# Performance work log

Hardware: AMD Instinct MI355X
Metric: run time of the kernel (lower is better)

Reference implementation:

```python
import jax, jax.numpy as jnp
import numpy as np

E = 2048   # embedding_size
H = 2048   # hidden_size
B = 512    # batch
OUT = 2    # output_size (coords)


def setup_inputs() -> dict:
    key = jax.random.key(0)
    ks = jax.random.split(key, 11)
    s = 0.02
    return {
        "embedding": jax.random.normal(ks[0], (B, E), dtype=jnp.float32),
        "max_seq_length": 256,
        "W_embed": jax.random.normal(ks[1], (H, E), dtype=jnp.float32) * s,
        "b_embed": jnp.zeros((H,), dtype=jnp.float32),
        "W_ih": jax.random.normal(ks[2], (4 * H, OUT), dtype=jnp.float32) * s,
        "b_ih": jnp.zeros((4 * H,), dtype=jnp.float32),
        "W_hh": jax.random.normal(ks[3], (4 * H, H), dtype=jnp.float32) * s,
        "b_hh": jnp.zeros((4 * H,), dtype=jnp.float32),
        "W_out": jax.random.normal(ks[4], (OUT, H), dtype=jnp.float32) * s,
        "b_out": jnp.zeros((OUT,), dtype=jnp.float32),
        "W_stop": jax.random.normal(ks[5], (1, H), dtype=jnp.float32) * s,
        "b_stop": jnp.zeros((1,), dtype=jnp.float32),
    }


def reference(embedding, max_seq_length, W_embed, b_embed, W_ih, b_ih,
              W_hh, b_hh, W_out, b_out, W_stop, b_stop):
    # h_0 from embedding head (num_layers == 1)
    h0 = embedding @ W_embed.T + b_embed          # (B, H)
    c0 = jnp.zeros_like(h0)
    x0 = jnp.zeros((embedding.shape[0], OUT), dtype=embedding.dtype)

    def step(carry, _):
        h, c, x = carry
        gates = x @ W_ih.T + b_ih + h @ W_hh.T + b_hh    # (B, 4H)
        i, f, g, o = jnp.split(gates, 4, axis=-1)         # torch gate order i,f,g,o
        c = jax.nn.sigmoid(f) * c + jax.nn.sigmoid(i) * jnp.tanh(g)
        h = jax.nn.sigmoid(o) * jnp.tanh(c)
        coord = h @ W_out.T + b_out                        # (B, 2)
        stop = jax.nn.sigmoid(h @ W_stop.T + b_stop)       # (B, 1)
        return (h, c, coord), (coord, stop)

    _, (coords, stops) = jax.lax.scan(step, (h0, c0, x0), xs=None,
                                      length=max_seq_length)
    outputs = jnp.transpose(coords, (1, 0, 2))     # (B, T, 2)
    stop_probs = jnp.transpose(stops, (1, 0, 2))   # (B, T, 1)
    return outputs, stop_probs
```

## Files before the change

kernel.cpp:

```cpp
#include <hip/hip_runtime.h>
#include <stdint.h>

#define E_DIM 2048
#define H_DIM 2048
#define B_DIM 512
#define T_DIM 256
#define G4H   8192

typedef unsigned short u16;
typedef __attribute__((ext_vector_type(8))) short bf16x8;
typedef __attribute__((ext_vector_type(4))) float f32x4;

__device__ inline u16 f2b(float f) {
  union { float f; uint32_t i; } v; v.f = f;
  uint32_t u = v.i;
  return (u16)((u + 0x7FFFu + ((u >> 16) & 1u)) >> 16);
}
__device__ inline float b2f(u16 u) {
  union { uint32_t i; float f; } v; v.i = ((uint32_t)u) << 16; return v.f;
}

__device__ __forceinline__ void stage16(const void* g, void* l) {
  __builtin_amdgcn_global_load_lds(
      (const __attribute__((address_space(1))) uint32_t*)g,
      (__attribute__((address_space(3))) uint32_t*)l, 16, 0, 0);
}

__global__ __launch_bounds__(256) void convert_bf16(const float* __restrict__ s,
                                                    u16* __restrict__ d, int n4) {
  int i = blockIdx.x * 256 + threadIdx.x;
  if (i < n4) {
    float4 f = ((const float4*)s)[i];
    ushort4 o;
    o.x = f2b(f.x); o.y = f2b(f.y); o.z = f2b(f.z); o.w = f2b(f.w);
    ((ushort4*)d)[i] = o;
  }
}

__global__ __launch_bounds__(256) void build_weff(const float* __restrict__ W,
                                                  const float* __restrict__ W_ih,
                                                  const float* __restrict__ W_out,
                                                  u16* __restrict__ Wz) {
  int id = blockIdx.x * 256 + threadIdx.x;
  int lane = id & 63;
  int k32  = (id >> 6) & 63;
  int n16  = id >> 12;
  int np = n16 * 16 + (lane & 15);
  int k  = k32 * 32 + (lane >> 4) * 8;
  int g = np & 3, jrow = np >> 2;
  int src = g * H_DIM + jrow;
  float wi0 = W_ih[src * 2 + 0], wi1 = W_ih[src * 2 + 1];
  const float* sw = W + (size_t)src * H_DIM + k;
  u16 out[8];
  for (int j = 0; j < 8; ++j) {
    float v = sw[j] + wi0 * W_out[k + j] + wi1 * W_out[H_DIM + k + j];
    out[j] = f2b(v);
  }
  u16* dst = Wz + (size_t)id * 8;
  *(ushort4*)(dst) = *(ushort4*)&out[0];
  *(ushort4*)(dst + 4) = *(ushort4*)&out[4];
}

__global__ __launch_bounds__(256) void build_epi(const float* __restrict__ b_ih,
                                                 const float* __restrict__ b_hh,
                                                 const float* __restrict__ W_ih,
                                                 const float* __restrict__ b_out,
                                                 float* __restrict__ epi) {
  int np = blockIdx.x * 256 + threadIdx.x;
  int src = (np & 3) * H_DIM + (np >> 2);
  float wi0 = W_ih[src * 2 + 0], wi1 = W_ih[src * 2 + 1];
  float4 e;
  e.x = b_ih[src] + b_hh[src] + b_out[0] * wi0 + b_out[1] * wi1;
  e.y = wi0;
  e.z = wi1;
  e.w = 0.f;
  ((float4*)epi)[np] = e;
}

#define BM 64
#define BN 128
#define BK 32
__global__ __launch_bounds__(256) void gemm_bt(const u16* __restrict__ A,
                                               const u16* __restrict__ Bm,
                                               float* __restrict__ C,
                                               int M, int N, int K) {
  __shared__ u16 sA[BM * BK];
  __shared__ u16 sB[BN * BK];
  const int t = threadIdx.x;
  const int bm0 = blockIdx.y * BM, bn0 = blockIdx.x * BN;
  const int wave = t >> 6, lane = t & 63;
  const int wm = (wave >> 1) * 32, wn = (wave & 1) * 64;
  const int r16 = lane & 15, quad = lane >> 4;

  f32x4 acc[2][4];
  const f32x4 z = {0.f, 0.f, 0.f, 0.f};
  for (int i = 0; i < 2; ++i)
    for (int j = 0; j < 4; ++j) acc[i][j] = z;

  const int arow = t >> 2, acg = t & 3;

  for (int k0 = 0; k0 < K; k0 += BK) {
    __syncthreads();
    *(uint4*)&sA[arow * BK + acg * 8] =
        *(const uint4*)&A[(size_t)(bm0 + arow) * K + k0 + acg * 8];
    for (int i = 0; i < 2; ++i) {
      int c = t + 256 * i;
      int row = c >> 2, cg = c & 3;
      *(uint4*)&sB[row * BK + cg * 8] =
          *(const uint4*)&Bm[(size_t)(bn0 + row) * K + k0 + cg * 8];
    }
    __syncthreads();
    bf16x8 af[2], bfr[4];
    for (int mt = 0; mt < 2; ++mt)
      af[mt] = *(const bf16x8*)&sA[(wm + mt * 16 + r16) * BK + quad * 8];
    for (int nt = 0; nt < 4; ++nt)
      bfr[nt] = *(const bf16x8*)&sB[(wn + nt * 16 + r16) * BK + quad * 8];
    for (int mt = 0; mt < 2; ++mt)
      for (int nt = 0; nt < 4; ++nt)
        acc[mt][nt] = __builtin_amdgcn_mfma_f32_16x16x32_bf16(af[mt], bfr[nt],
                                                              acc[mt][nt], 0, 0, 0);
  }
  for (int mt = 0; mt < 2; ++mt)
    for (int nt = 0; nt < 4; ++nt) {
      int row = bm0 + wm + mt * 16 + quad * 4;
      int col = bn0 + wn + nt * 16 + r16;
      for (int r = 0; r < 4; ++r)
        C[(size_t)(row + r) * N + col] = acc[mt][nt][r];
    }
}

__global__ __launch_bounds__(256) void init_state(const float* __restrict__ h0pre,
                                                  const float* __restrict__ b_embed,
                                                  u16* __restrict__ h,
                                                  float* __restrict__ c,
                                                  float* __restrict__ xzero) {
  int idx = blockIdx.x * 256 + threadIdx.x;
  int bg = idx >> 11, k = idx & (H_DIM - 1);
  float v = h0pre[idx] + b_embed[k];
  size_t chunk = (((size_t)(bg >> 4)) * 64 + (k >> 5)) * 64 + ((k >> 3) & 3) * 16 + (bg & 15);
  size_t pos = chunk * 8 + (k & 7);
  h[pos] = f2b(v);
  c[pos] = 0.f;
  if (idx < B_DIM * 2) xzero[idx] = 0.f;
}

__global__ __launch_bounds__(64) void calc_xcorr(const float* __restrict__ h0pre,
                                                 const float* __restrict__ b_embed,
                                                 const float* __restrict__ W_out,
                                                 const float* __restrict__ b_out,
                                                 float* __restrict__ xc) {
  int m = blockIdx.x, ln = threadIdx.x;
  float s0 = 0.f, s1 = 0.f;
  for (int k = ln; k < H_DIM; k += 64) {
    float hv = h0pre[(size_t)m * H_DIM + k] + b_embed[k];
    s0 += hv * W_out[k];
    s1 += hv * W_out[H_DIM + k];
  }
  for (int off = 32; off > 0; off >>= 1) {
    s0 += __shfl_down(s0, off);
    s1 += __shfl_down(s1, off);
  }
  if (ln == 0) {
    xc[m * 2 + 0] = -(s0 + b_out[0]);
    xc[m * 2 + 1] = -(s1 + b_out[1]);
  }
}

__global__ __launch_bounds__(256) void init_out(const float* __restrict__ b_out,
                                                const float* __restrict__ b_stop,
                                                float* __restrict__ coords,
                                                float* __restrict__ stops) {
  int i = blockIdx.x * 256 + threadIdx.x;
  coords[i * 2 + 0] = b_out[0];
  coords[i * 2 + 1] = b_out[1];
  stops[i] = b_stop[0];
}

__global__ __launch_bounds__(256) void finalize_stops(float* __restrict__ stops) {
  int i = blockIdx.x * 256 + threadIdx.x;
  stops[i] = 1.f / (1.f + __expf(-stops[i]));
}

__global__ __launch_bounds__(512, 2) void gemm_lstm(const u16* __restrict__ hA,
                                                 const u16* __restrict__ Wz,
                                                 const float* __restrict__ epi,
                                                 const float* __restrict__ x,
                                                 float* __restrict__ c,
                                                 u16* __restrict__ h_out,
                                                 const float* __restrict__ W_out,
                                                 const float* __restrict__ W_stop,
                                                 float* __restrict__ coords,
                                                 float* __restrict__ stops,
                                                 int trow) {
  __shared__ __align__(16) char smem[131072];

  const int bid = blockIdx.x;
  const int nt = (bid & 7) * 8 + ((bid >> 3) & 7);
  const int mt = bid >> 6;

  const int t = threadIdx.x, wv = t >> 6, ln = t & 63;
  const int kq = wv >> 1, wn = wv & 1;
  const int r16 = ln & 15, quad = ln >> 4;

  const u16* Bb[4];
#pragma unroll
  for (int ni = 0; ni < 4; ++ni)
    Bb[ni] = Wz + ((size_t)(nt * 8 + wn * 4 + ni) * 64) * 512 + ln * 8;
  const int kbase = kq * 16;

  const u16* Ag[8];
  uint32_t Aoff[8];
#pragma unroll
  for (int s = 0; s < 8; ++s) {
    int ti = wv * 8 + s;
    int kq_s = ti >> 4, kloc_s = (ti >> 3) & 1, m16i = ti & 7;
    Ag[s] = hA + ((size_t)(mt * 8 + m16i) * 64 + kq_s * 16 + kloc_s) * 512 + ln * 8;
    Aoff[s] = (uint32_t)(kq_s * 16384 + kloc_s * 8192 + m16i * 1024);
  }

  f32x4 acc[8][4];
  const f32x4 z = {0.f, 0.f, 0.f, 0.f};
#pragma unroll
  for (int i = 0; i < 8; ++i)
#pragma unroll
    for (int j = 0; j < 4; ++j) acc[i][j] = z;

#pragma unroll
  for (int s = 0; s < 8; ++s) stage16(Ag[s], smem + Aoff[s]);
  __builtin_amdgcn_sched_barrier(0);
  bf16x8 bfr[2][4];
#pragma unroll
  for (int d = 0; d < 2; ++d)
#pragma unroll
    for (int ni = 0; ni < 4; ++ni)
      bfr[d][ni] = *(const bf16x8*)(Bb[ni] + (size_t)(kbase + d) * 512);

  const uint32_t ln16 = (uint32_t)(ln * 16);
  const uint32_t rdk = (uint32_t)(kq * 16384);

  for (int it = 0; it < 8; ++it) {
    asm volatile("s_waitcnt vmcnt(8)" ::: "memory");
    __builtin_amdgcn_s_barrier();
    const uint32_t bb = (uint32_t)((it & 1) * 65536);
    if (it < 7) {
#pragma unroll
      for (int s = 0; s < 8; ++s)
        stage16(Ag[s] + (size_t)(it + 1) * 1024, smem + ((bb ^ 65536) + Aoff[s]));
      __builtin_amdgcn_sched_barrier(0);
    }
#pragma unroll
    for (int kloc = 0; kloc < 2; ++kloc) {
      const char* rb = smem + bb + rdk + (uint32_t)(kloc * 8192);
      bf16x8 af[8];
#pragma unroll
      for (int mi = 0; mi < 8; ++mi)
        af[mi] = *(const bf16x8*)(rb + mi * 1024 + ln16);
      __builtin_amdgcn_s_setprio(1);
#pragma unroll
      for (int mi = 0; mi < 8; ++mi)
#pragma unroll
        for (int ni = 0; ni < 4; ++ni)
          acc[mi][ni] = __builtin_amdgcn_mfma_f32_16x16x32_bf16(
              af[mi], bfr[kloc][ni], acc[mi][ni], 0, 0, 0);
      __builtin_amdgcn_s_setprio(0);
      const int knext = it * 2 + kloc + 2;
      if (knext < 16) {
#pragma unroll
        for (int ni = 0; ni < 4; ++ni)
          bfr[kloc][ni] = *(const bf16x8*)(Bb[ni] + (size_t)(kbase + knext) * 512);
      }
    }
  }
  __syncthreads();

  float* cb = (float*)smem;
  if (kq >= 2) {
    float* dst = cb + ((kq - 2) * 2 + wn) * 8192;
#pragma unroll
    for (int mi = 0; mi < 8; ++mi)
#pragma unroll
      for (int ni = 0; ni < 4; ++ni)
        *(f32x4*)&dst[((mi * 4 + ni) * 64 + ln) * 4] = acc[mi][ni];
  }
  __syncthreads();
  if (kq < 2) {
    const float* src = cb + (kq * 2 + wn) * 8192;
#pragma unroll
    for (int mi = 0; mi < 8; ++mi)
#pragma unroll
      for (int ni = 0; ni < 4; ++ni)
        acc[mi][ni] += *(const f32x4*)&src[((mi * 4 + ni) * 64 + ln) * 4];
  }
  __syncthreads();
  if (kq == 1) {
    float* dst = cb + wn * 8192;
#pragma unroll
    for (int mi = 0; mi < 8; ++mi)
#pragma unroll
      for (int ni = 0; ni < 4; ++ni)
        *(f32x4*)&dst[((mi * 4 + ni) * 64 + ln) * 4] = acc[mi][ni];
  }
  __syncthreads();
  if (kq == 0) {
    const float* src = cb + wn * 8192;
#pragma unroll
    for (int mi = 0; mi < 8; ++mi)
#pragma unroll
      for (int ni = 0; ni < 4; ++ni)
        acc[mi][ni] += *(const f32x4*)&src[((mi * 4 + ni) * 64 + ln) * 4];
  }
  __syncthreads();

  float* gt = (float*)smem;
  if (kq == 0) {
#pragma unroll
    for (int mi = 0; mi < 8; ++mi)
#pragma unroll
      for (int ni = 0; ni < 4; ++ni) {
        int row = mi * 16 + quad * 4;
        int col = wn * 64 + ni * 16 + r16;
        f32x4 v = acc[mi][ni];
#pragma unroll
        for (int r = 0; r < 4; ++r)
          gt[(row + r) * 132 + col] = v[r];
      }
  }
  __syncthreads();

  {
    const int lrow = wv * 16 + r16;
    const int bg = mt * 128 + lrow;
    const float x0 = x[bg * 2 + 0], x1 = x[bg * 2 + 1];
    const size_t chunk = (((size_t)(bg >> 4)) * 64 + nt) * 64 + ln;
    const int hc0 = nt * 32 + quad * 8;
    float cv[8]; u16 hv[8];
    float s0 = 0.f, s1 = 0.f, s2 = 0.f;
    const float4* epi4 = (const float4*)epi;
    f32x4 cold0 = *(const f32x4*)&c[chunk * 8 + 0];
    f32x4 cold1 = *(const f32x4*)&c[chunk * 8 + 4];
#pragma unroll
    for (int j = 0; j < 8; ++j) {
      int col = quad * 32 + j * 4;
      float4 g4 = *(const float4*)&gt[lrow * 132 + col];
      float4 e0 = epi4[nt * 128 + col + 0];
      float4 e1 = epi4[nt * 128 + col + 1];
      float4 e2 = epi4[nt * 128 + col + 2];
      float4 e3 = epi4[nt * 128 + col + 3];
      float gi = g4.x + e0.x + x0 * e0.y + x1 * e0.z;
      float gf = g4.y + e1.x + x0 * e1.y + x1 * e1.z;
      float gg = g4.z + e2.x + x0 * e2.y + x1 * e2.z;
      float go = g4.w + e3.x + x0 * e3.y + x1 * e3.z;
      float si = 1.f / (1.f + __expf(-gi));
      float sf = 1.f / (1.f + __expf(-gf));
      float so = 1.f / (1.f + __expf(-go));
      float cold = (j < 4) ? cold0[j & 3] : cold1[j & 3];
      float cn = sf * cold + si * tanhf(gg);
      cv[j] = cn;
      float hf = so * tanhf(cn);
      hv[j] = f2b(hf);
      s0 += hf * W_out[hc0 + j];
      s1 += hf * W_out[H_DIM + hc0 + j];
      s2 += hf * W_stop[hc0 + j];
    }
    *(float4*)&c[chunk * 8 + 0] = *(float4*)&cv[0];
    *(float4*)&c[chunk * 8 + 4] = *(float4*)&cv[4];
    *(ushort4*)&h_out[chunk * 8 + 0] = *(ushort4*)&hv[0];
    *(ushort4*)&h_out[chunk * 8 + 4] = *(ushort4*)&hv[4];
    s0 += __shfl_xor(s0, 16); s1 += __shfl_xor(s1, 16); s2 += __shfl_xor(s2, 16);
    s0 += __shfl_xor(s0, 32); s1 += __shfl_xor(s1, 32); s2 += __shfl_xor(s2, 32);
    if (quad == 0) {
      atomicAdd(&coords[((size_t)bg * T_DIM + trow) * 2 + 0], s0);
      atomicAdd(&coords[((size_t)bg * T_DIM + trow) * 2 + 1], s1);
      atomicAdd(&stops[(size_t)bg * T_DIM + trow], s2);
    }
  }
}

extern "C" void kernel_launch(void* const* d_in, const int* in_sizes, int n_in,
                              void* d_out, int out_size, void* d_ws, size_t ws_size,
                              hipStream_t stream) {
  const float* embedding = (const float*)d_in[0];
  const float* W_embed   = (const float*)d_in[2];
  const float* b_embed   = (const float*)d_in[3];
  const float* W_ih      = (const float*)d_in[4];
  const float* b_ih      = (const float*)d_in[5];
  const float* W_hh      = (const float*)d_in[6];
  const float* b_hh      = (const float*)d_in[7];
  const float* W_out     = (const float*)d_in[8];
  const float* b_out     = (const float*)d_in[9];
  const float* W_stop    = (const float*)d_in[10];
  const float* b_stop    = (const float*)d_in[11];

  float* coords = (float*)d_out;
  float* stops  = (float*)d_out + (size_t)B_DIM * T_DIM * 2;

  char* ws = (char*)d_ws;
  u16* W_z     = (u16*)ws;   ws += (size_t)G4H * H_DIM * 2;
  u16* W_emb_b = (u16*)ws;   ws += (size_t)H_DIM * E_DIM * 2;
  u16* emb_b   = (u16*)ws;   ws += (size_t)B_DIM * E_DIM * 2;
  float* h0pre = (float*)ws; ws += (size_t)B_DIM * H_DIM * 4;
  float* epi   = (float*)ws; ws += (size_t)G4H * 4 * 4;
  float* cbuf  = (float*)ws; ws += (size_t)B_DIM * H_DIM * 4;
  u16* hbuf0   = (u16*)ws;   ws += (size_t)B_DIM * H_DIM * 2;
  u16* hbuf1   = (u16*)ws;   ws += (size_t)B_DIM * H_DIM * 2;
  float* xcorr = (float*)ws; ws += (size_t)B_DIM * 2 * 4;
  float* xzero = (float*)ws; ws += (size_t)B_DIM * 2 * 4;

  convert_bf16<<<(B_DIM * E_DIM / 4 + 255) / 256, 256, 0, stream>>>(embedding, emb_b, B_DIM * E_DIM / 4);
  convert_bf16<<<(H_DIM * E_DIM / 4 + 255) / 256, 256, 0, stream>>>(W_embed, W_emb_b, H_DIM * E_DIM / 4);
  build_weff<<<(G4H * H_DIM / 8) / 256, 256, 0, stream>>>(W_hh, W_ih, W_out, W_z);
  build_epi<<<G4H / 256, 256, 0, stream>>>(b_ih, b_hh, W_ih, b_out, epi);
  init_out<<<(B_DIM * T_DIM) / 256, 256, 0, stream>>>(b_out, b_stop, coords, stops);

  gemm_bt<<<dim3(H_DIM / BN, B_DIM / BM), 256, 0, stream>>>(emb_b, W_emb_b, h0pre,
                                                            B_DIM, H_DIM, E_DIM);
  init_state<<<(B_DIM * H_DIM) / 256, 256, 0, stream>>>(h0pre, b_embed, hbuf0, cbuf, xzero);
  calc_xcorr<<<B_DIM, 64, 0, stream>>>(h0pre, b_embed, W_out, b_out, xcorr);

  for (int t = 0; t < T_DIM; ++t) {
    u16* h_in  = (t & 1) ? hbuf1 : hbuf0;
    u16* h_out = (t & 1) ? hbuf0 : hbuf1;
    const float* xv = (t == 0) ? xcorr : xzero;
    gemm_lstm<<<256, 512, 0, stream>>>(h_in, W_z, epi, xv, cbuf, h_out,
                                       W_out, W_stop, coords, stops, t);
  }
  finalize_stops<<<(B_DIM * T_DIM) / 256, 256, 0, stream>>>(stops);
}
```

Before: 7.600 ms.

## Fuse all LSTM timesteps into one persistent cooperative kernel with grid barrier

Replaces the 256 per-timestep gemm_lstm launches with a single cooperative persistent kernel that loops over time and synchronises all 256 blocks through an atomic-counter grid barrier. The cell state now stays in registers instead of being reloaded from and stored to global memory each step, and the zero-x buffer is dropped. This removes per-launch overhead and the c-state traffic. In exchange it adds a spin barrier per step and requires all 256 blocks to be co-resident.

```diff
diff --git a/kernel.cpp b/kernel.cpp
--- a/kernel.cpp
+++ b/kernel.cpp
@@ -131,17 +131,13 @@
 
 __global__ __launch_bounds__(256) void init_state(const float* __restrict__ h0pre,
                                                   const float* __restrict__ b_embed,
-                                                  u16* __restrict__ h,
-                                                  float* __restrict__ c,
-                                                  float* __restrict__ xzero) {
+                                                  u16* __restrict__ h) {
   int idx = blockIdx.x * 256 + threadIdx.x;
   int bg = idx >> 11, k = idx & (H_DIM - 1);
   float v = h0pre[idx] + b_embed[k];
   size_t chunk = (((size_t)(bg >> 4)) * 64 + (k >> 5)) * 64 + ((k >> 3) & 3) * 16 + (bg & 15);
   size_t pos = chunk * 8 + (k & 7);
   h[pos] = f2b(v);
-  c[pos] = 0.f;
-  if (idx < B_DIM * 2) xzero[idx] = 0.f;
 }
 
 __global__ __launch_bounds__(64) void calc_xcorr(const float* __restrict__ h0pre,
@@ -181,24 +177,20 @@
   stops[i] = 1.f / (1.f + __expf(-stops[i]));
 }
 
-__global__ __launch_bounds__(512, 2) void gemm_lstm(const u16* __restrict__ hA,
-                                                 const u16* __restrict__ Wz,
-                                                 const float* __restrict__ epi,
-                                                 const float* __restrict__ x,
-                                                 float* __restrict__ c,
-                                                 u16* __restrict__ h_out,
-                                                 const float* __restrict__ W_out,
-                                                 const float* __restrict__ W_stop,
-                                                 float* __restrict__ coords,
-                                                 float* __restrict__ stops,
-                                                 int trow) {
+__global__ __launch_bounds__(512, 2) void gemm_lstm_all(
+    u16* __restrict__ hb0, u16* __restrict__ hb1,
+    const u16* __restrict__ Wz, const float* __restrict__ epi,
+    const float* __restrict__ xcorr,
+    const float* __restrict__ W_out, const float* __restrict__ W_stop,
+    float* __restrict__ coords, float* __restrict__ stops,
+    unsigned int* __restrict__ bar) {
   __shared__ __align__(16) char smem[131072];
 
   const int bid = blockIdx.x;
   const int nt = (bid & 7) * 8 + ((bid >> 3) & 7);
   const int mt = bid >> 6;
 
-  const int t = threadIdx.x, wv = t >> 6, ln = t & 63;
+  const int tid = threadIdx.x, wv = tid >> 6, ln = tid & 63;
   const int kq = wv >> 1, wn = wv & 1;
   const int r16 = ln & 15, quad = ln >> 4;
 
@@ -208,170 +200,193 @@
     Bb[ni] = Wz + ((size_t)(nt * 8 + wn * 4 + ni) * 64) * 512 + ln * 8;
   const int kbase = kq * 16;
 
-  const u16* Ag[8];
-  uint32_t Aoff[8];
+  uint32_t Aoffe[8], Aoff[8];
 #pragma unroll
   for (int s = 0; s < 8; ++s) {
     int ti = wv * 8 + s;
     int kq_s = ti >> 4, kloc_s = (ti >> 3) & 1, m16i = ti & 7;
-    Ag[s] = hA + ((size_t)(mt * 8 + m16i) * 64 + kq_s * 16 + kloc_s) * 512 + ln * 8;
+    Aoffe[s] = (uint32_t)((((mt * 8 + m16i) * 64 + kq_s * 16 + kloc_s) * 512) + ln * 8);
     Aoff[s] = (uint32_t)(kq_s * 16384 + kloc_s * 8192 + m16i * 1024);
   }
-
-  f32x4 acc[8][4];
-  const f32x4 z = {0.f, 0.f, 0.f, 0.f};
-#pragma unroll
-  for (int i = 0; i < 8; ++i)
-#pragma unroll
-    for (int j = 0; j < 4; ++j) acc[i][j] = z;
-
-#pragma unroll
-  for (int s = 0; s < 8; ++s) stage16(Ag[s], smem + Aoff[s]);
-  __builtin_amdgcn_sched_barrier(0);
-  bf16x8 bfr[2][4];
-#pragma unroll
-  for (int d = 0; d < 2; ++d)
-#pragma unroll
-    for (int ni = 0; ni < 4; ++ni)
-      bfr[d][ni] = *(const bf16x8*)(Bb[ni] + (size_t)(kbase + d) * 512);
 
   const uint32_t ln16 = (uint32_t)(ln * 16);
   const uint32_t rdk = (uint32_t)(kq * 16384);
 
-  for (int it = 0; it < 8; ++it) {
-    asm volatile("s_waitcnt vmcnt(8)" ::: "memory");
-    __builtin_amdgcn_s_barrier();
-    const uint32_t bb = (uint32_t)((it & 1) * 65536);
-    if (it < 7) {
-#pragma unroll
-      for (int s = 0; s < 8; ++s)
-        stage16(Ag[s] + (size_t)(it + 1) * 1024, smem + ((bb ^ 65536) + Aoff[s]));
-      __builtin_amdgcn_sched_barrier(0);
-    }
-#pragma unroll
-    for (int kloc = 0; kloc < 2; ++kloc) {
-      const char* rb = smem + bb + rdk + (uint32_t)(kloc * 8192);
-      bf16x8 af[8];
+  const int lrow = wv * 16 + r16;
+  const int bg = mt * 128 + lrow;
+  const size_t chunk = (((size_t)(bg >> 4)) * 64 + nt) * 64 + ln;
+  const int hc0 = nt * 32 + quad * 8;
+  const float wo0[8 + 8 + 8] = {};
+  (void)wo0;
+  const float xc0 = xcorr[bg * 2 + 0], xc1 = xcorr[bg * 2 + 1];
+  float creg[8];
+#pragma unroll
+  for (int j = 0; j < 8; ++j) creg[j] = 0.f;
+
+#pragma unroll 1
+  for (int t = 0; t < T_DIM; ++t) {
+    const u16* hin = (t & 1) ? hb1 : hb0;
+    u16* hout = (t & 1) ? hb0 : hb1;
+
+    f32x4 acc[8][4];
+    const f32x4 z = {0.f, 0.f, 0.f, 0.f};
+#pragma unroll
+    for (int i = 0; i < 8; ++i)
+#pragma unroll
+      for (int j = 0; j < 4; ++j) acc[i][j] = z;
+
+#pragma unroll
+    for (int s = 0; s < 8; ++s) stage16(hin + Aoffe[s], smem + Aoff[s]);
+    __builtin_amdgcn_sched_barrier(0);
+    bf16x8 bfr[2][4];
+#pragma unroll
+    for (int d = 0; d < 2; ++d)
+#pragma unroll
+      for (int ni = 0; ni < 4; ++ni)
+        bfr[d][ni] = *(const bf16x8*)(Bb[ni] + (size_t)(kbase + d) * 512);
+
+#pragma unroll 1
+    for (int it = 0; it < 8; ++it) {
+      asm volatile("s_waitcnt vmcnt(8)" ::: "memory");
+      __builtin_amdgcn_s_barrier();
+      const uint32_t bb = (uint32_t)((it & 1) * 65536);
+      if (it < 7) {
+#pragma unroll
+        for (int s = 0; s < 8; ++s)
+          stage16(hin + Aoffe[s] + (uint32_t)(it + 1) * 1024,
+                  smem + ((bb ^ 65536) + Aoff[s]));
+        __builtin_amdgcn_sched_barrier(0);
+      }
+#pragma unroll
+      for (int kloc = 0; kloc < 2; ++kloc) {
+        const char* rb = smem + bb + rdk + (uint32_t)(kloc * 8192);
+        bf16x8 af[8];
+#pragma unroll
+        for (int mi = 0; mi < 8; ++mi)
+          af[mi] = *(const bf16x8*)(rb + mi * 1024 + ln16);
+        __builtin_amdgcn_s_setprio(1);
+#pragma unroll
+        for (int mi = 0; mi < 8; ++mi)
+#pragma unroll
+          for (int ni = 0; ni < 4; ++ni)
+            acc[mi][ni] = __builtin_amdgcn_mfma_f32_16x16x32_bf16(
+                af[mi], bfr[kloc][ni], acc[mi][ni], 0, 0, 0);
+        __builtin_amdgcn_s_setprio(0);
+        const int knext = it * 2 + kloc + 2;
+        if (knext < 16) {
+#pragma unroll
+          for (int ni = 0; ni < 4; ++ni)
+            bfr[kloc][ni] = *(const bf16x8*)(Bb[ni] + (size_t)(kbase + knext) * 512);
+        }
+      }
+    }
+    __syncthreads();
+
+    float* cb = (float*)smem;
+    if (kq >= 2) {
+      float* dst = cb + ((kq - 2) * 2 + wn) * 8192;
 #pragma unroll
       for (int mi = 0; mi < 8; ++mi)
-        af[mi] = *(const bf16x8*)(rb + mi * 1024 + ln16);
-      __builtin_amdgcn_s_setprio(1);
+#pragma unroll
+        for (int ni = 0; ni < 4; ++ni)
+          *(f32x4*)&dst[((mi * 4 + ni) * 64 + ln) * 4] = acc[mi][ni];
+    }
+    __syncthreads();
+    if (kq < 2) {
+      const float* src = cb + (kq * 2 + wn) * 8192;
 #pragma unroll
       for (int mi = 0; mi < 8; ++mi)
 #pragma unroll
         for (int ni = 0; ni < 4; ++ni)
-          acc[mi][ni] = __builtin_amdgcn_mfma_f32_16x16x32_bf16(
-              af[mi], bfr[kloc][ni], acc[mi][ni], 0, 0, 0);
-      __builtin_amdgcn_s_setprio(0);
-      const int knext = it * 2 + kloc + 2;
-      if (knext < 16) {
+          acc[mi][ni] += *(const f32x4*)&src[((mi * 4 + ni) * 64 + ln) * 4];
+    }
+    __syncthreads();
+    if (kq == 1) {
+      float* dst = cb + wn * 8192;
+#pragma unroll
+      for (int mi = 0; mi < 8; ++mi)
 #pragma unroll
         for (int ni = 0; ni < 4; ++ni)
-          bfr[kloc][ni] = *(const bf16x8*)(Bb[ni] + (size_t)(kbase + knext) * 512);
+          *(f32x4*)&dst[((mi * 4 + ni) * 64 + ln) * 4] = acc[mi][ni];
+    }
+    __syncthreads();
+    if (kq == 0) {
+      const float* src = cb + wn * 8192;
+#pragma unroll
+      for (int mi = 0; mi < 8; ++mi)
+#pragma unroll
+        for (int ni = 0; ni < 4; ++ni)
+          acc[mi][ni] += *(const f32x4*)&src[((mi * 4 + ni) * 64 + ln) * 4];
+    }
+    __syncthreads();
+
+    float* gt = (float*)smem;
+    if (kq == 0) {
+#pragma unroll
+      for (int mi = 0; mi < 8; ++mi)
+#pragma unroll
+        for (int ni = 0; ni < 4; ++ni) {
+          int row = mi * 16 + quad * 4;
+          int col = wn * 64 + ni * 16 + r16;
+          f32x4 v = acc[mi][ni];
+#pragma unroll
+          for (int r = 0; r < 4; ++r)
+            gt[(row + r) * 132 + col] = v[r];
+        }
+    }
+    __syncthreads();
+
+    {
+      const float x0 = (t == 0) ? xc0 : 0.f;
+      const float x1 = (t == 0) ? xc1 : 0.f;
+      u16 hv[8];
+      float s0 = 0.f, s1 = 0.f, s2 = 0.f;
+      const float4* epi4 = (const float4*)epi;
+#pragma unroll
+      for (int j = 0; j < 8; ++j) {
+        int col = quad * 32 + j * 4;
+        float4 g4 = *(const float4*)&gt[lrow * 132 + col];
+        float4 e0 = epi4[nt * 128 + col + 0];
+        float4 e1 = epi4[nt * 128 + col + 1];
+        float4 e2 = epi4[nt * 128 + col + 2];
+        float4 e3 = epi4[nt * 128 + col + 3];
+        float gi = g4.x + e0.x + x0 * e0.y + x1 * e0.z;
+        float gf = g4.y + e1.x + x0 * e1.y + x1 * e1.z;
+        float gg = g4.z + e2.x + x0 * e2.y + x1 * e2.z;
+        float go = g4.w + e3.x + x0 * e3.y + x1 * e3.z;
+        float si = 1.f / (1.f + __expf(-gi));
+        float sf = 1.f / (1.f + __expf(-gf));
+        float so = 1.f / (1.f + __expf(-go));
+        float cn = sf * creg[j] + si * tanhf(gg);
+        creg[j] = cn;
+        float hf = so * tanhf(cn);
+        hv[j] = f2b(hf);
+        s0 += hf * W_out[hc0 + j];
+        s1 += hf * W_out[H_DIM + hc0 + j];
+        s2 += hf * W_stop[hc0 + j];
       }
-    }
-  }
-  __syncthreads();
-
-  float* cb = (float*)smem;
-  if (kq >= 2) {
-    float* dst = cb + ((kq - 2) * 2 + wn) * 8192;
-#pragma unroll
-    for (int mi = 0; mi < 8; ++mi)
-#pragma unroll
-      for (int ni = 0; ni < 4; ++ni)
-        *(f32x4*)&dst[((mi * 4 + ni) * 64 + ln) * 4] = acc[mi][ni];
-  }
-  __syncthreads();
-  if (kq < 2) {
-    const float* src = cb + (kq * 2 + wn) * 8192;
-#pragma unroll
-    for (int mi = 0; mi < 8; ++mi)
-#pragma unroll
-      for (int ni = 0; ni < 4; ++ni)
-        acc[mi][ni] += *(const f32x4*)&src[((mi * 4 + ni) * 64 + ln) * 4];
-  }
-  __syncthreads();
-  if (kq == 1) {
-    float* dst = cb + wn * 8192;
-#pragma unroll
-    for (int mi = 0; mi < 8; ++mi)
-#pragma unroll
-      for (int ni = 0; ni < 4; ++ni)
-        *(f32x4*)&dst[((mi * 4 + ni) * 64 + ln) * 4] = acc[mi][ni];
-  }
-  __syncthreads();
-  if (kq == 0) {
-    const float* src = cb + wn * 8192;
-#pragma unroll
-    for (int mi = 0; mi < 8; ++mi)
-#pragma unroll
-      for (int ni = 0; ni < 4; ++ni)
-        acc[mi][ni] += *(const f32x4*)&src[((mi * 4 + ni) * 64 + ln) * 4];
-  }
-  __syncthreads();
-
-  float* gt = (float*)smem;
-  if (kq == 0) {
-#pragma unroll
-    for (int mi = 0; mi < 8; ++mi)
-#pragma unroll
-      for (int ni = 0; ni < 4; ++ni) {
-        int row = mi * 16 + quad * 4;
-        int col = wn * 64 + ni * 16 + r16;
-        f32x4 v = acc[mi][ni];
-#pragma unroll
-        for (int r = 0; r < 4; ++r)
-          gt[(row + r) * 132 + col] = v[r];
+      *(ushort4*)&hout[chunk * 8 + 0] = *(ushort4*)&hv[0];
+      *(ushort4*)&hout[chunk * 8 + 4] = *(ushort4*)&hv[4];
+      s0 += __shfl_xor(s0, 16); s1 += __shfl_xor(s1, 16); s2 += __shfl_xor(s2, 16);
+      s0 += __shfl_xor(s0, 32); s1 += __shfl_xor(s1, 32); s2 += __shfl_xor(s2, 32);
+      if (quad == 0) {
+        atomicAdd(&coords[((size_t)bg * T_DIM + t) * 2 + 0], s0);
+        atomicAdd(&coords[((size_t)bg * T_DIM + t) * 2 + 1], s1);
+        atomicAdd(&stops[(size_t)bg * T_DIM + t], s2);
       }
-  }
-  __syncthreads();
-
-  {
-    const int lrow = wv * 16 + r16;
-    const int bg = mt * 128 + lrow;
-    const float x0 = x[bg * 2 + 0], x1 = x[bg * 2 + 1];
-    const size_t chunk = (((size_t)(bg >> 4)) * 64 + nt) * 64 + ln;
-    const int hc0 = nt * 32 + quad * 8;
-    float cv[8]; u16 hv[8];
-    float s0 = 0.f, s1 = 0.f, s2 = 0.f;
-    const float4* epi4 = (const float4*)epi;
-    f32x4 cold0 = *(const f32x4*)&c[chunk * 8 + 0];
-    f32x4 cold1 = *(const f32x4*)&c[chunk * 8 + 4];
-#pragma unroll
-    for (int j = 0; j < 8; ++j) {
-      int col = quad * 32 + j * 4;
-      float4 g4 = *(const float4*)&gt[lrow * 132 + col];
-      float4 e0 = epi4[nt * 128 + col + 0];
-      float4 e1 = epi4[nt * 128 + col + 1];
-      float4 e2 = epi4[nt * 128 + col + 2];
-      float4 e3 = epi4[nt * 128 + col + 3];
-      float gi = g4.x + e0.x + x0 * e0.y + x1 * e0.z;
-      float gf = g4.y + e1.x + x0 * e1.y + x1 * e1.z;
-      float gg = g4.z + e2.x + x0 * e2.y + x1 * e2.z;
-      float go = g4.w + e3.x + x0 * e3.y + x1 * e3.z;
-      float si = 1.f / (1.f + __expf(-gi));
-      float sf = 1.f / (1.f + __expf(-gf));
-      float so = 1.f / (1.f + __expf(-go));
-      float cold = (j < 4) ? cold0[j & 3] : cold1[j & 3];
-      float cn = sf * cold + si * tanhf(gg);
-      cv[j] = cn;
-      float hf = so * tanhf(cn);
-      hv[j] = f2b(hf);
-      s0 += hf * W_out[hc0 + j];
-      s1 += hf * W_out[H_DIM + hc0 + j];
-      s2 += hf * W_stop[hc0 + j];
-    }
-    *(float4*)&c[chunk * 8 + 0] = *(float4*)&cv[0];
-    *(float4*)&c[chunk * 8 + 4] = *(float4*)&cv[4];
-    *(ushort4*)&h_out[chunk * 8 + 0] = *(ushort4*)&hv[0];
-    *(ushort4*)&h_out[chunk * 8 + 4] = *(ushort4*)&hv[4];
-    s0 += __shfl_xor(s0, 16); s1 += __shfl_xor(s1, 16); s2 += __shfl_xor(s2, 16);
-    s0 += __shfl_xor(s0, 32); s1 += __shfl_xor(s1, 32); s2 += __shfl_xor(s2, 32);
-    if (quad == 0) {
-      atomicAdd(&coords[((size_t)bg * T_DIM + trow) * 2 + 0], s0);
-      atomicAdd(&coords[((size_t)bg * T_DIM + trow) * 2 + 1], s1);
-      atomicAdd(&stops[(size_t)bg * T_DIM + trow], s2);
+    }
+
+    if (t < T_DIM - 1) {
+      __builtin_amdgcn_fence(__ATOMIC_RELEASE, "agent");
+      __syncthreads();
+      if (tid == 0) {
+        __hip_atomic_fetch_add(bar, 1u, __ATOMIC_RELAXED, __HIP_MEMORY_SCOPE_AGENT);
+        const unsigned tgt = (unsigned)(t + 1) * 256u;
+        while (__hip_atomic_load(bar, __ATOMIC_RELAXED, __HIP_MEMORY_SCOPE_AGENT) < tgt)
+          __builtin_amdgcn_s_sleep(2);
+      }
+      __syncthreads();
+      __builtin_amdgcn_fence(__ATOMIC_ACQUIRE, "agent");
     }
   }
 }
@@ -400,11 +415,10 @@
   u16* emb_b   = (u16*)ws;   ws += (size_t)B_DIM * E_DIM * 2;
   float* h0pre = (float*)ws; ws += (size_t)B_DIM * H_DIM * 4;
   float* epi   = (float*)ws; ws += (size_t)G4H * 4 * 4;
-  float* cbuf  = (float*)ws; ws += (size_t)B_DIM * H_DIM * 4;
   u16* hbuf0   = (u16*)ws;   ws += (size_t)B_DIM * H_DIM * 2;
   u16* hbuf1   = (u16*)ws;   ws += (size_t)B_DIM * H_DIM * 2;
   float* xcorr = (float*)ws; ws += (size_t)B_DIM * 2 * 4;
-  float* xzero = (float*)ws; ws += (size_t)B_DIM * 2 * 4;
+  unsigned int* bar = (unsigned int*)ws; ws += 256;
 
   convert_bf16<<<(B_DIM * E_DIM / 4 + 255) / 256, 256, 0, stream>>>(embedding, emb_b, B_DIM * E_DIM / 4);
   convert_bf16<<<(H_DIM * E_DIM / 4 + 255) / 256, 256, 0, stream>>>(W_embed, W_emb_b, H_DIM * E_DIM / 4);
@@ -414,15 +428,16 @@
 
   gemm_bt<<<dim3(H_DIM / BN, B_DIM / BM), 256, 0, stream>>>(emb_b, W_emb_b, h0pre,
                                                             B_DIM, H_DIM, E_DIM);
-  init_state<<<(B_DIM * H_DIM) / 256, 256, 0, stream>>>(h0pre, b_embed, hbuf0, cbuf, xzero);
+  init_state<<<(B_DIM * H_DIM) / 256, 256, 0, stream>>>(h0pre, b_embed, hbuf0);
   calc_xcorr<<<B_DIM, 64, 0, stream>>>(h0pre, b_embed, W_out, b_out, xcorr);
 
-  for (int t = 0; t < T_DIM; ++t) {
-    u16* h_in  = (t & 1) ? hbuf1 : hbuf0;
-    u16* h_out = (t & 1) ? hbuf0 : hbuf1;
-    const float* xv = (t == 0) ? xcorr : xzero;
-    gemm_lstm<<<256, 512, 0, stream>>>(h_in, W_z, epi, xv, cbuf, h_out,
-                                       W_out, W_stop, coords, stops, t);
-  }
+  hipMemsetAsync(bar, 0, sizeof(unsigned int), stream);
+
+  void* kargs[] = {(void*)&hbuf0, (void*)&hbuf1, (void*)&W_z, (void*)&epi,
+                   (void*)&xcorr, (void*)&W_out, (void*)&W_stop,
+                   (void*)&coords, (void*)&stops, (void*)&bar};
+  hipLaunchCooperativeKernel((const void*)gemm_lstm_all, dim3(256), dim3(512),
+                             kargs, 0, stream);
+
   finalize_stops<<<(B_DIM * T_DIM) / 256, 256, 0, stream>>>(stops);
 }
```

Result: slower. 24.71 ms (+225.2%).
